# Performance work log

Hardware: AMD Instinct MI355X
Metric: run time of the kernel (lower is better)

Reference implementation:

```python
import jax, jax.numpy as jnp
import numpy as np

K_OVERGEN = 3
BETA = 0.75


def _point_sample(feat, coords):
    """feat: [B,C,H,W]; coords: [B,N,2] in [0,1], (x,y) order.
    Equivalent to F.grid_sample(feat, 2*coords-1, mode='bilinear',
    padding_mode='zeros', align_corners=False) -> returns [B,C,N]."""
    B, C, H, W = feat.shape
    g = 2.0 * coords - 1.0
    # align_corners=False unnormalization
    x = ((g[..., 0] + 1.0) * W - 1.0) * 0.5  # [B,N]
    y = ((g[..., 1] + 1.0) * H - 1.0) * 0.5
    x0 = jnp.floor(x)
    y0 = jnp.floor(y)
    wx1 = x - x0
    wy1 = y - y0
    bidx = jnp.arange(B)[:, None]  # [B,1]

    def gather(yi, xi):
        # zero padding for out-of-range corners
        valid = (xi >= 0) & (xi <= W - 1) & (yi >= 0) & (yi <= H - 1)
        xc = jnp.clip(xi, 0, W - 1).astype(jnp.int32)
        yc = jnp.clip(yi, 0, H - 1).astype(jnp.int32)
        v = feat[bidx, :, yc, xc]  # [B,N,C]
        return v * valid[..., None].astype(feat.dtype)

    v00 = gather(y0, x0)
    v01 = gather(y0, x0 + 1.0)
    v10 = gather(y0 + 1.0, x0)
    v11 = gather(y0 + 1.0, x0 + 1.0)
    out = (v00 * ((1.0 - wy1) * (1.0 - wx1))[..., None]
           + v01 * ((1.0 - wy1) * wx1)[..., None]
           + v10 * (wy1 * (1.0 - wx1))[..., None]
           + v11 * (wy1 * wx1)[..., None])  # [B,N,C]
    return jnp.transpose(out, (0, 2, 1))  # [B,C,N]


def _sampling_points(out, N, over_generation, coverage):
    # sort class scores per pixel, descending (uncertainty = -(top1 - top2))
    mask_sorted = -jnp.sort(-out, axis=1)  # [B,C,H,W]
    og_map = _point_sample(mask_sorted, over_generation)  # [B,C,k*N]
    uncertainty = -(og_map[:, 0] - og_map[:, 1])  # [B,k*N]
    n_imp = int(BETA * N)
    _, idx = jax.lax.top_k(uncertainty, n_imp)  # [B,n_imp]
    importance = jnp.take_along_axis(over_generation, idx[..., None], axis=1)
    return jnp.concatenate([importance, coverage], axis=1)  # [B,N,2]


def setup_inputs() -> dict:
    key = jax.random.key(0)
    ks = jax.random.split(key, 7)
    x = jax.random.normal(ks[0], (8, 3, 1024, 1024), dtype=jnp.float32)
    res2 = jax.random.normal(ks[1], (8, 512, 256, 256), dtype=jnp.float32)
    out = jax.random.normal(ks[2], (8, 2, 64, 64), dtype=jnp.float32)
    over_generation = jax.random.uniform(ks[3], (8, 192, 2), dtype=jnp.float32)
    coverage = jax.random.uniform(ks[4], (8, 16, 2), dtype=jnp.float32)
    w = jax.random.normal(ks[5], (2, 514), dtype=jnp.float32) * 0.05
    b = jax.random.normal(ks[6], (2,), dtype=jnp.float32) * 0.05
    return {"x": x, "res2": res2, "out": out,
            "over_generation": over_generation, "coverage": coverage,
            "w": w, "b": b}


def reference(x, res2, out, over_generation, coverage, w, b):
    N = x.shape[-1] // 16  # points on a stride-16 map of the input
    points = _sampling_points(out, N, over_generation, coverage)  # [B,N,2]
    coarse = _point_sample(out, points)   # [B,2,N]
    fine = _point_sample(res2, points)    # [B,512,N]
    feat = jnp.concatenate([coarse, fine], axis=1)  # [B,514,N]
    # 1x1 Conv1d == per-point linear
    rend = jnp.einsum('oc,bcn->bon', w, feat) + b[None, :, None]  # [B,2,N]
    return rend, points
```

## Files before the change

### kernel.cpp

```cpp
#include <hip/hip_runtime.h>


__device__ __forceinline__ void bilin_setup(float px, float py, int H, int W,
                                            int idx[4], float cw[4]) {
    float gx = 2.0f * px - 1.0f;
    float gy = 2.0f * py - 1.0f;
    float x = ((gx + 1.0f) * (float)W - 1.0f) * 0.5f;
    float y = ((gy + 1.0f) * (float)H - 1.0f) * 0.5f;
    float x0 = floorf(x), y0 = floorf(y);
    float wx1 = x - x0, wy1 = y - y0;
    float wxs[2] = {1.0f - wx1, wx1};
    float wys[2] = {1.0f - wy1, wy1};
    float xs[2] = {x0, x0 + 1.0f};
    float ys[2] = {y0, y0 + 1.0f};
#pragma unroll
    for (int dy = 0; dy < 2; ++dy) {
#pragma unroll
        for (int dx = 0; dx < 2; ++dx) {
            float xf = xs[dx], yf = ys[dy];
            bool valid = (xf >= 0.0f) && (xf <= (float)(W - 1)) &&
                         (yf >= 0.0f) && (yf <= (float)(H - 1));
            float xc = fminf(fmaxf(xf, 0.0f), (float)(W - 1));
            float yc = fminf(fmaxf(yf, 0.0f), (float)(H - 1));
            int xi = (int)xc, yi = (int)yc;
            idx[dy * 2 + dx] = yi * W + xi;
            cw[dy * 2 + dx] = valid ? (wys[dy] * wxs[dx]) : 0.0f;
        }
    }
}

__global__ void k_points(const float* __restrict__ outm,
                         const float* __restrict__ og,
                         const float* __restrict__ cov,
                         float* __restrict__ points) {
    const int b = blockIdx.x;
    const int t = threadIdx.x;
    __shared__ float u[192];
    if (t < 192) {
        float px = og[(b * 192 + t) * 2 + 0];
        float py = og[(b * 192 + t) * 2 + 1];
        int idx[4];
        float cw[4];
        bilin_setup(px, py, 64, 64, idx, cw);
        const float* c0 = outm + ((size_t)b * 2 + 0) * 4096;
        const float* c1 = outm + ((size_t)b * 2 + 1) * 4096;
        float s0 = 0.0f, s1 = 0.0f;
#pragma unroll
        for (int k = 0; k < 4; ++k) {
            float a = c0[idx[k]];
            float d = c1[idx[k]];
            s0 += fmaxf(a, d) * cw[k];
            s1 += fminf(a, d) * cw[k];
        }
        u[t] = s1 - s0;
    }
    __syncthreads();
    if (t < 192) {
        float ui = u[t];
        int rank = 0;
        for (int j = 0; j < 192; ++j) {
            float uj = u[j];
            if (uj > ui || (uj == ui && j < t)) rank++;
        }
        if (rank < 48) {
            points[b * 128 + rank * 2 + 0] = og[(b * 192 + t) * 2 + 0];
            points[b * 128 + rank * 2 + 1] = og[(b * 192 + t) * 2 + 1];
        }
    }
    if (t < 16) {
        points[b * 128 + (48 + t) * 2 + 0] = cov[(b * 16 + t) * 2 + 0];
        points[b * 128 + (48 + t) * 2 + 1] = cov[(b * 16 + t) * 2 + 1];
    }
}

__global__ void k_render(const float* __restrict__ outm,
                         const float* __restrict__ res2,
                         const float* __restrict__ w,
                         const float* __restrict__ bias,
                         const float* __restrict__ points,
                         float* __restrict__ rend) {
    const int b = blockIdx.x >> 6;
    const int n = blockIdx.x & 63;
    const int t = threadIdx.x;
    const float px = points[b * 128 + n * 2 + 0];
    const float py = points[b * 128 + n * 2 + 1];
    int idx[4];
    float cw[4];
    bilin_setup(px, py, 256, 256, idx, cw);
    float acc0 = 0.0f, acc1 = 0.0f;
#pragma unroll
    for (int cc = 0; cc < 2; ++cc) {
        int c = t + cc * 256;
        const float* base = res2 + ((size_t)b * 512 + c) * 65536;
        float f = base[idx[0]] * cw[0] + base[idx[1]] * cw[1] +
                  base[idx[2]] * cw[2] + base[idx[3]] * cw[3];
        acc0 += w[2 + c] * f;
        acc1 += w[514 + 2 + c] * f;
    }
    __shared__ float s0[256], s1[256];
    s0[t] = acc0;
    s1[t] = acc1;
    __syncthreads();
    for (int off = 128; off > 0; off >>= 1) {
        if (t < off) {
            s0[t] += s0[t + off];
            s1[t] += s1[t + off];
        }
        __syncthreads();
    }
    if (t == 0) {
        int idc[4];
        float cwc[4];
        bilin_setup(px, py, 64, 64, idc, cwc);
        const float* c0p = outm + ((size_t)b * 2 + 0) * 4096;
        const float* c1p = outm + ((size_t)b * 2 + 1) * 4096;
        float coarse0 = c0p[idc[0]] * cwc[0] + c0p[idc[1]] * cwc[1] +
                        c0p[idc[2]] * cwc[2] + c0p[idc[3]] * cwc[3];
        float coarse1 = c1p[idc[0]] * cwc[0] + c1p[idc[1]] * cwc[1] +
                        c1p[idc[2]] * cwc[2] + c1p[idc[3]] * cwc[3];
        float r0 = w[0] * coarse0 + w[1] * coarse1 + s0[0] + bias[0];
        float r1 = w[514] * coarse0 + w[514 + 1] * coarse1 + s1[0] + bias[1];
        rend[((size_t)b * 2 + 0) * 64 + n] = r0;
        rend[((size_t)b * 2 + 1) * 64 + n] = r1;
    }
}

extern "C" void kernel_launch(void* const* d_in, const int* in_sizes, int n_in,
                              void* d_out, int out_size, void* d_ws, size_t ws_size,
                              hipStream_t stream) {
    const float* res2 = (const float*)d_in[1];
    const float* outm = (const float*)d_in[2];
    const float* og   = (const float*)d_in[3];
    const float* cov  = (const float*)d_in[4];
    const float* w    = (const float*)d_in[5];
    const float* bias = (const float*)d_in[6];

    float* rend = (float*)d_out;
    float* points = rend + 1024;

    k_points<<<8, 256, 0, stream>>>(outm, og, cov, points);
    k_render<<<512, 256, 0, stream>>>(outm, res2, w, bias, points, rend);
}
```

Measured before the change: 25.15 us.

## Fuse point selection into render kernel with redundant per-block ranking

Merges the point-selection kernel into the render kernel. Each block recomputes the uncertainty and rank of all 192 over-generated points for its batch and keeps the point whose rank equals its own index, which removes the second launch and the dependency on points written to global memory. The block grows to 512 threads, one channel each, and the shared-memory tree reduction becomes wave shuffles followed by a small cross-wave sum. The cost is 48x redundant ranking work per batch, done by every block.

```diff
diff --git a/kernel.cpp b/kernel.cpp
--- a/kernel.cpp
+++ b/kernel.cpp
@@ -29,99 +29,110 @@
     }
 }
 
-__global__ void k_points(const float* __restrict__ outm,
-                         const float* __restrict__ og,
-                         const float* __restrict__ cov,
-                         float* __restrict__ points) {
-    const int b = blockIdx.x;
-    const int t = threadIdx.x;
-    __shared__ float u[192];
-    if (t < 192) {
-        float px = og[(b * 192 + t) * 2 + 0];
-        float py = og[(b * 192 + t) * 2 + 1];
-        int idx[4];
-        float cw[4];
-        bilin_setup(px, py, 64, 64, idx, cw);
-        const float* c0 = outm + ((size_t)b * 2 + 0) * 4096;
-        const float* c1 = outm + ((size_t)b * 2 + 1) * 4096;
-        float s0 = 0.0f, s1 = 0.0f;
-#pragma unroll
-        for (int k = 0; k < 4; ++k) {
-            float a = c0[idx[k]];
-            float d = c1[idx[k]];
-            s0 += fmaxf(a, d) * cw[k];
-            s1 += fminf(a, d) * cw[k];
-        }
-        u[t] = s1 - s0;
-    }
-    __syncthreads();
-    if (t < 192) {
-        float ui = u[t];
-        int rank = 0;
-        for (int j = 0; j < 192; ++j) {
-            float uj = u[j];
-            if (uj > ui || (uj == ui && j < t)) rank++;
-        }
-        if (rank < 48) {
-            points[b * 128 + rank * 2 + 0] = og[(b * 192 + t) * 2 + 0];
-            points[b * 128 + rank * 2 + 1] = og[(b * 192 + t) * 2 + 1];
-        }
-    }
-    if (t < 16) {
-        points[b * 128 + (48 + t) * 2 + 0] = cov[(b * 16 + t) * 2 + 0];
-        points[b * 128 + (48 + t) * 2 + 1] = cov[(b * 16 + t) * 2 + 1];
-    }
-}
-
-__global__ void k_render(const float* __restrict__ outm,
-                         const float* __restrict__ res2,
-                         const float* __restrict__ w,
-                         const float* __restrict__ bias,
-                         const float* __restrict__ points,
-                         float* __restrict__ rend) {
+__global__ __launch_bounds__(512) void k_fused(
+    const float* __restrict__ outm,
+    const float* __restrict__ res2,
+    const float* __restrict__ w,
+    const float* __restrict__ bias,
+    const float* __restrict__ og,
+    const float* __restrict__ cov,
+    float* __restrict__ rend,
+    float* __restrict__ points) {
     const int b = blockIdx.x >> 6;
     const int n = blockIdx.x & 63;
     const int t = threadIdx.x;
-    const float px = points[b * 128 + n * 2 + 0];
-    const float py = points[b * 128 + n * 2 + 1];
+
+    __shared__ float u[192];
+    __shared__ float sp[2];
+
+    if (n < 48) {
+        if (t < 192) {
+            float2 p = ((const float2*)og)[b * 192 + t];
+            int idx[4];
+            float cw[4];
+            bilin_setup(p.x, p.y, 64, 64, idx, cw);
+            const float* c0 = outm + (size_t)b * 2 * 4096;
+            const float* c1 = c0 + 4096;
+            float s0 = 0.0f, s1 = 0.0f;
+#pragma unroll
+            for (int k = 0; k < 4; ++k) {
+                float a = c0[idx[k]];
+                float d = c1[idx[k]];
+                s0 += fmaxf(a, d) * cw[k];
+                s1 += fminf(a, d) * cw[k];
+            }
+            u[t] = s1 - s0;
+        }
+        __syncthreads();
+        if (t < 192) {
+            float ui = u[t];
+            int rank = 0;
+            for (int j = 0; j < 192; ++j) {
+                float uj = u[j];
+                rank += (uj > ui || (uj == ui && j < t)) ? 1 : 0;
+            }
+            if (rank == n) {
+                float2 p = ((const float2*)og)[b * 192 + t];
+                sp[0] = p.x;
+                sp[1] = p.y;
+            }
+        }
+        __syncthreads();
+    } else {
+        if (t == 0) {
+            float2 p = ((const float2*)cov)[b * 16 + (n - 48)];
+            sp[0] = p.x;
+            sp[1] = p.y;
+        }
+        __syncthreads();
+    }
+
+    const float px = sp[0], py = sp[1];
+    if (t == 0) {
+        points[b * 128 + n * 2 + 0] = px;
+        points[b * 128 + n * 2 + 1] = py;
+    }
+
     int idx[4];
     float cw[4];
     bilin_setup(px, py, 256, 256, idx, cw);
-    float acc0 = 0.0f, acc1 = 0.0f;
+    const int c = t;
+    const float* base = res2 + ((size_t)b * 512 + c) * 65536;
+    float f = base[idx[0]] * cw[0] + base[idx[1]] * cw[1] +
+              base[idx[2]] * cw[2] + base[idx[3]] * cw[3];
+    float acc0 = w[2 + c] * f;
+    float acc1 = w[516 + c] * f;
+
 #pragma unroll
-    for (int cc = 0; cc < 2; ++cc) {
-        int c = t + cc * 256;
-        const float* base = res2 + ((size_t)b * 512 + c) * 65536;
-        float f = base[idx[0]] * cw[0] + base[idx[1]] * cw[1] +
-                  base[idx[2]] * cw[2] + base[idx[3]] * cw[3];
-        acc0 += w[2 + c] * f;
-        acc1 += w[514 + 2 + c] * f;
+    for (int off = 32; off > 0; off >>= 1) {
+        acc0 += __shfl_down(acc0, off, 64);
+        acc1 += __shfl_down(acc1, off, 64);
     }
-    __shared__ float s0[256], s1[256];
-    s0[t] = acc0;
-    s1[t] = acc1;
+    __shared__ float r0s[8], r1s[8];
+    const int wid = t >> 6, lane = t & 63;
+    if (lane == 0) {
+        r0s[wid] = acc0;
+        r1s[wid] = acc1;
+    }
     __syncthreads();
-    for (int off = 128; off > 0; off >>= 1) {
-        if (t < off) {
-            s0[t] += s0[t + off];
-            s1[t] += s1[t + off];
+    if (t == 0) {
+        float a0 = 0.0f, a1 = 0.0f;
+#pragma unroll
+        for (int i = 0; i < 8; ++i) {
+            a0 += r0s[i];
+            a1 += r1s[i];
         }
-        __syncthreads();
-    }
-    if (t == 0) {
         int idc[4];
         float cwc[4];
         bilin_setup(px, py, 64, 64, idc, cwc);
-        const float* c0p = outm + ((size_t)b * 2 + 0) * 4096;
-        const float* c1p = outm + ((size_t)b * 2 + 1) * 4096;
+        const float* c0p = outm + (size_t)b * 2 * 4096;
+        const float* c1p = c0p + 4096;
         float coarse0 = c0p[idc[0]] * cwc[0] + c0p[idc[1]] * cwc[1] +
                         c0p[idc[2]] * cwc[2] + c0p[idc[3]] * cwc[3];
         float coarse1 = c1p[idc[0]] * cwc[0] + c1p[idc[1]] * cwc[1] +
                         c1p[idc[2]] * cwc[2] + c1p[idc[3]] * cwc[3];
-        float r0 = w[0] * coarse0 + w[1] * coarse1 + s0[0] + bias[0];
-        float r1 = w[514] * coarse0 + w[514 + 1] * coarse1 + s1[0] + bias[1];
-        rend[((size_t)b * 2 + 0) * 64 + n] = r0;
-        rend[((size_t)b * 2 + 1) * 64 + n] = r1;
+        rend[((size_t)b * 2 + 0) * 64 + n] = w[0] * coarse0 + w[1] * coarse1 + a0 + bias[0];
+        rend[((size_t)b * 2 + 1) * 64 + n] = w[514] * coarse0 + w[515] * coarse1 + a1 + bias[1];
     }
 }
 
@@ -138,6 +149,5 @@
     float* rend = (float*)d_out;
     float* points = rend + 1024;
 
-    k_points<<<8, 256, 0, stream>>>(outm, og, cov, points);
-    k_render<<<512, 256, 0, stream>>>(outm, res2, w, bias, points, rend);
+    k_fused<<<512, 512, 0, stream>>>(outm, res2, w, bias, og, cov, rend, points);
 }
```

After: 21.19 us. 1.19x faster.
